# Optimization experiments

Measured on AMD Instinct MI355X. Metric: run time of the kernel, lower is better.

The kernel has to match this reference:

```python
import jax, jax.numpy as jnp
import numpy as np

# Product-key memory config (matches init_kwargs)
HEADS = 4
K_DIM = 512          # per-head query/key dim; split in two halves of 256
HALF = K_DIM // 2
V_DIM = 512
SUBSIZE = 512        # sub-keys per bank; value table size = SUBSIZE**2
SIZE = SUBSIZE * SUBSIZE
TOPK = 8
TEMP = 1.0
B, T = 4, 2048


def setup_inputs() -> dict:
    key = jax.random.key(0)
    kq, kk, kv = jax.random.split(key, 3)
    bound = 1.0 / np.sqrt(K_DIM)  # reset_parameters: uniform(-1/sqrt(k_dim), 1/sqrt(k_dim))
    query = jax.random.normal(kq, (B, T, HEADS * K_DIM), dtype=jnp.float32)
    keys = jax.random.uniform(kk, (2 * HEADS * SUBSIZE, HALF), dtype=jnp.float32,
                              minval=-bound, maxval=bound)
    # reset_parameters: normal(0, v_dim**-0.5)
    values = jax.random.normal(kv, (SIZE, V_DIM), dtype=jnp.float32) * (V_DIM ** -0.5)
    return {"query": query, "keys": keys, "values": values}


def reference(query, keys, values):
    """retrieve_values: product-key two-stage topk + softmax-weighted embedding bag.
    query: [B, T, HEADS*K_DIM]; keys: [2*HEADS*SUBSIZE, HALF]; values: [SIZE, V_DIM]
    returns retrieved values [B*T, V_DIM].
    """
    Bq, Tq = query.shape[:2]
    N = Bq * Tq
    q = query.reshape(N, HEADS, K_DIM)
    q1, q2 = q[..., :HALF], q[..., HALF:]
    k = keys.reshape(2, HEADS, SUBSIZE, HALF)

    # Sub-key score matmuls (the two 'cdist-like' searches)
    s1 = jnp.einsum('nhd,hsd->nhs', q1, k[0])       # [N, H, SUBSIZE]
    s2 = jnp.einsum('nhd,hsd->nhs', q2, k[1])       # [N, H, SUBSIZE]

    ts1, ti1 = jax.lax.top_k(s1, TOPK)               # [N, H, TOPK]
    ts2, ti2 = jax.lax.top_k(s2, TOPK)

    # Cartesian combination of the two topk sets, then global topk
    comb = (ts1[..., :, None] + ts2[..., None, :]).reshape(N, HEADS, TOPK * TOPK)
    scores, flat_idx = jax.lax.top_k(comb, TOPK)     # [N, H, TOPK]
    sel1 = jnp.take_along_axis(ti1, flat_idx // TOPK, axis=-1)
    sel2 = jnp.take_along_axis(ti2, flat_idx % TOPK, axis=-1)
    indices = sel1 * SUBSIZE + sel2                  # global value-table indices [N, H, TOPK]

    # score_transform: softmax over heads*topk (score_nonlinear='softmax')
    w = jax.nn.softmax(scores.reshape(N, HEADS * TOPK) / TEMP, axis=-1)

    # xformers_embedding_bag: weighted gather-sum over the huge value table
    gathered = values[indices.reshape(N, HEADS * TOPK)]   # [N, H*TOPK, V_DIM]
    vals = jnp.einsum('nk,nkd->nd', w, gathered)          # [N, V_DIM]
    return vals
```

## Files before the change

### kernel.cpp

```cpp
#include <hip/hip_runtime.h>
#include <hip/hip_bf16.h>
#include <math.h>

typedef unsigned short u16;
typedef __attribute__((ext_vector_type(8))) short short8;
typedef __attribute__((ext_vector_type(4))) float f32x4;

#define N_TOK   8192
#define N_HEADS 4
#define KDIM    512
#define HALFD   256
#define VDIM    512
#define SUBK    512
#define NCAND   16

__device__ __forceinline__ u16 f2bf(float f) {
    unsigned u = __float_as_uint(f);
    u += 0x7fffu + ((u >> 16) & 1u);
    return (u16)(u >> 16);
}

__device__ __forceinline__ unsigned med3u(unsigned a, unsigned b, unsigned c) {
    unsigned d;
    asm("v_med3_u32 %0, %1, %2, %3" : "=v"(d) : "v"(a), "v"(b), "v"(c));
    return d;
}

__global__ void k_convert(const float* __restrict__ in, u16* __restrict__ out, int n4) {
    int i = blockIdx.x * blockDim.x + threadIdx.x;
    int stride = gridDim.x * blockDim.x;
    for (; i < n4; i += stride) {
        float4 v = ((const float4*)in)[i];
        unsigned a = (unsigned)f2bf(v.x) | ((unsigned)f2bf(v.y) << 16);
        unsigned b = (unsigned)f2bf(v.z) | ((unsigned)f2bf(v.w) << 16);
        ((uint2*)out)[i] = make_uint2(a, b);
    }
}

__global__ __launch_bounds__(256) void k_score_topk(
    const float* __restrict__ query,
    const u16* __restrict__ kb,
    int* __restrict__ cand)
{
    __shared__ unsigned sc[16 * 513];
    const int nb = blockIdx.x, h = blockIdx.y, half = blockIdx.z;
    const int tid = threadIdx.x;
    const int wave = tid >> 6, l = tid & 63;
    const int lr = l & 15, lk = l >> 4;

    const float* qbase = query + (size_t)(nb * 16 + lr) * (N_HEADS * KDIM)
                       + h * KDIM + half * HALFD + lk * 8;
    short8 a[8];
#pragma unroll
    for (int kf = 0; kf < 8; ++kf) {
        float4 q0 = *(const float4*)(qbase + kf * 32);
        float4 q1 = *(const float4*)(qbase + kf * 32 + 4);
        short8 t;
        t[0] = (short)f2bf(q0.x); t[1] = (short)f2bf(q0.y);
        t[2] = (short)f2bf(q0.z); t[3] = (short)f2bf(q0.w);
        t[4] = (short)f2bf(q1.x); t[5] = (short)f2bf(q1.y);
        t[6] = (short)f2bf(q1.z); t[7] = (short)f2bf(q1.w);
        a[kf] = t;
    }

    const u16* kbase = kb + (size_t)(half * N_HEADS + h) * SUBK * HALFD;
#pragma unroll
    for (int t = 0; t < 8; ++t) {
        const int st = wave * 8 + t;
        const u16* kp = kbase + (size_t)(st * 16 + lr) * HALFD + lk * 8;
        short8 b[8];
#pragma unroll
        for (int kf = 0; kf < 8; ++kf)
            b[kf] = *(const short8*)(kp + kf * 32);
        f32x4 acc = {0.f, 0.f, 0.f, 0.f};
#pragma unroll
        for (int kf = 0; kf < 8; ++kf)
            acc = __builtin_amdgcn_mfma_f32_16x16x32_bf16(a[kf], b[kf], acc, 0, 0, 0);
#pragma unroll
        for (int r = 0; r < 4; ++r) {
            unsigned ub = __float_as_uint(acc[r]);
            unsigned key = ub ^ ((unsigned)((int)ub >> 31) | 0x80000000u);
            key = (key & 0xFFFFFE00u) | (unsigned)(st * 16 + lr);
            sc[(lk * 4 + r) * 513 + st * 16 + lr] = key;
        }
    }
    __syncthreads();

    const int row = tid >> 4, sub = tid & 15;
    unsigned tv[NCAND];
#pragma unroll
    for (int j = 0; j < NCAND; ++j) tv[j] = 0u;
    const int base = row * 513 + sub;
#pragma unroll
    for (int t = 0; t < 32; ++t) {
        unsigned v = sc[base + (t << 4)];
#pragma unroll
        for (int j = NCAND - 1; j >= 1; --j)
            tv[j] = med3u(tv[j - 1], tv[j], v);
        tv[0] = (tv[0] > v) ? tv[0] : v;
    }

    unsigned keep = 0;
#pragma unroll
    for (int r = 0; r < NCAND; ++r) {
        unsigned w = tv[0];
#pragma unroll
        for (int d = 1; d < 16; d <<= 1) {
            unsigned o = __shfl_xor(w, d, 16);
            w = (o > w) ? o : w;
        }
        if (sub == r) keep = w;
        bool pop = (tv[0] == w);
#pragma unroll
        for (int j = 0; j < NCAND - 1; ++j) tv[j] = pop ? tv[j + 1] : tv[j];
        tv[NCAND - 1] = pop ? 0u : tv[NCAND - 1];
    }
    const int n = nb * 16 + row;
    cand[((size_t)n * 8 + (h * 2 + half)) * NCAND + sub] = (int)(keep & 0x1FFu);
}

__global__ __launch_bounds__(256) void k_select(
    const float* __restrict__ query,
    const float* __restrict__ keys,
    const int* __restrict__ cand,
    int* __restrict__ gout,
    float* __restrict__ wout)
{
    __shared__ double rv[8][16];
    __shared__ int    ri[8][16];
    __shared__ double tsv[8][8];
    __shared__ int    tsi[8][8];
    __shared__ double s_comb[32];
    __shared__ int    sgi[32];

    const int n = blockIdx.x;
    const int tid = threadIdx.x;

    {
        const int dot = tid >> 1, pt = tid & 1;
        const int g = dot >> 4, j = dot & 15;
        const int h = g >> 1, half = g & 1;
        const int sidx = cand[((size_t)n * 8 + g) * NCAND + j];
        const float* qrow = query + (size_t)n * (N_HEADS * KDIM) + h * KDIM + half * HALFD + pt * 128;
        const float* krow = keys + ((size_t)(half * N_HEADS + h) * SUBK + sidx) * HALFD + pt * 128;
        double a0 = 0, a1 = 0, a2 = 0, a3 = 0;
#pragma unroll 8
        for (int d = 0; d < 128; d += 4) {
            float4 qv = *(const float4*)(qrow + d);
            float4 kv = *(const float4*)(krow + d);
            a0 = fma((double)qv.x, (double)kv.x, a0);
            a1 = fma((double)qv.y, (double)kv.y, a1);
            a2 = fma((double)qv.z, (double)kv.z, a2);
            a3 = fma((double)qv.w, (double)kv.w, a3);
        }
        double s = (a0 + a1) + (a2 + a3);
        double o = __shfl_xor(s, 1);
        if (pt == 0) { rv[g][j] = s + o; ri[g][j] = sidx; }
    }
    __syncthreads();

    if (tid < 128) {
        const int g = tid >> 4, j = tid & 15;
        double v = rv[g][j];
        const int idx = ri[g][j];
        for (int r = 0; r < 8; ++r) {
            double bv = v; int bj = j;
#pragma unroll
            for (int d = 1; d < 16; d <<= 1) {
                double ov = __shfl_xor(bv, d, 16);
                int    oj = __shfl_xor(bj, d, 16);
                if (ov > bv || (ov == bv && oj < bj)) { bv = ov; bj = oj; }
            }
            int widx = __shfl(idx, bj, 16);
            if (j == r) { tsv[g][r] = bv; tsi[g][r] = widx; }
            if (j == bj) v = -1e300;
        }
    }
    __syncthreads();

    {
        const int h = tid >> 6, f = tid & 63;
        double c = tsv[h * 2][f >> 3] + tsv[h * 2 + 1][f & 7];
        for (int r = 0; r < 8; ++r) {
            double bv = c; int bf = f;
#pragma unroll
            for (int d = 1; d < 64; d <<= 1) {
                double ov = __shfl_xor(bv, d, 64);
                int    of = __shfl_xor(bf, d, 64);
                if (ov > bv || (ov == bv && of < bf)) { bv = ov; bf = of; }
            }
            if (f == r) {
                s_comb[h * 8 + r] = bv;
                sgi[h * 8 + r] = tsi[h * 2][bf >> 3] * SUBK + tsi[h * 2 + 1][bf & 7];
            }
            if (f == bf) c = -1e300;
        }
    }
    __syncthreads();

    if (tid < 32) {
        const int k = tid;
        double s = s_comb[k];
        double m = s;
#pragma unroll
        for (int d = 1; d < 32; d <<= 1) m = fmax(m, __shfl_xor(m, d, 32));
        float e = expf((float)(s - m));
        float sum = e;
#pragma unroll
        for (int d = 1; d < 32; d <<= 1) sum += __shfl_xor(sum, d, 32);
        wout[(size_t)n * 32 + k] = e / sum;
        gout[(size_t)n * 32 + k] = sgi[k];
    }
}

__global__ __launch_bounds__(256) void k_gather(
    const float* __restrict__ values,
    const int* __restrict__ gidx,
    const float* __restrict__ w,
    float* __restrict__ out)
{
    const int tok = blockIdx.x * 4 + (threadIdx.x >> 6);
    const int lane = threadIdx.x & 63;

    float wv = 0.f; unsigned off = 0u;
    if (lane < 32) {
        wv  = w[(size_t)tok * 32 + lane];
        off = (unsigned)gidx[(size_t)tok * 32 + lane] * (unsigned)VDIM;
    }

    float4 acc0 = {0.f, 0.f, 0.f, 0.f};
    float4 acc1 = {0.f, 0.f, 0.f, 0.f};
#pragma unroll
    for (int kb = 0; kb < 32; kb += 8) {
        float4 v0[8], v1[8];
#pragma unroll
        for (int r = 0; r < 8; ++r) {
            unsigned o = (unsigned)__shfl((int)off, kb + r, 64);
            const float* vr = values + (size_t)o;
            v0[r] = *(const float4*)(vr + lane * 4);
            v1[r] = *(const float4*)(vr + 256 + lane * 4);
        }
#pragma unroll
        for (int r = 0; r < 8; ++r) {
            const float wk = __shfl(wv, kb + r, 64);
            acc0.x = fmaf(wk, v0[r].x, acc0.x);
            acc0.y = fmaf(wk, v0[r].y, acc0.y);
            acc0.z = fmaf(wk, v0[r].z, acc0.z);
            acc0.w = fmaf(wk, v0[r].w, acc0.w);
            acc1.x = fmaf(wk, v1[r].x, acc1.x);
            acc1.y = fmaf(wk, v1[r].y, acc1.y);
            acc1.z = fmaf(wk, v1[r].z, acc1.z);
            acc1.w = fmaf(wk, v1[r].w, acc1.w);
        }
    }
    float* orow = out + (size_t)tok * VDIM;
    *(float4*)(orow + lane * 4) = acc0;
    *(float4*)(orow + 256 + lane * 4) = acc1;
}

extern "C" void kernel_launch(void* const* d_in, const int* in_sizes, int n_in,
                              void* d_out, int out_size, void* d_ws, size_t ws_size,
                              hipStream_t stream) {
    const float* query  = (const float*)d_in[0];
    const float* keys   = (const float*)d_in[1];
    const float* values = (const float*)d_in[2];
    float* out = (float*)d_out;

    char* ws = (char*)d_ws;
    u16* kb    = (u16*)ws;
    int* cand  = (int*)(ws + 2097152);
    int* gidxb = (int*)(ws + 2097152 + 4194304);
    float* wb  = (float*)(ws + 2097152 + 4194304 + 1048576);

    k_convert<<<512, 256, 0, stream>>>(keys, kb, (2 * N_HEADS * SUBK * HALFD) / 4);

    dim3 gB(N_TOK / 16, N_HEADS, 2);
    k_score_topk<<<gB, 256, 0, stream>>>(query, kb, cand);

    k_select<<<N_TOK, 256, 0, stream>>>(query, keys, cand, gidxb, wb);
    k_gather<<<N_TOK / 4, 256, 0, stream>>>(values, gidxb, wb, out);
}
```

Measured before the change: 416.3 us.

## Process two tokens per wave and gather values in index-range passes

```diff
diff --git a/kernel.cpp b/kernel.cpp
--- a/kernel.cpp
+++ b/kernel.cpp
@@ -219,43 +219,57 @@
     const float* __restrict__ w,
     float* __restrict__ out)
 {
-    const int tok = blockIdx.x * 4 + (threadIdx.x >> 6);
+    const int wid = blockIdx.x * 4 + (threadIdx.x >> 6);
     const int lane = threadIdx.x & 63;
-
-    float wv = 0.f; unsigned off = 0u;
+    const int t0 = wid * 2, t1 = t0 + 1;
+
+    float wv0 = 0.f, wv1 = 0.f;
+    unsigned r0 = 0xFFFFFFFFu, r1 = 0xFFFFFFFFu;
     if (lane < 32) {
-        wv  = w[(size_t)tok * 32 + lane];
-        off = (unsigned)gidx[(size_t)tok * 32 + lane] * (unsigned)VDIM;
-    }
-
-    float4 acc0 = {0.f, 0.f, 0.f, 0.f};
-    float4 acc1 = {0.f, 0.f, 0.f, 0.f};
-#pragma unroll
-    for (int kb = 0; kb < 32; kb += 8) {
-        float4 v0[8], v1[8];
-#pragma unroll
-        for (int r = 0; r < 8; ++r) {
-            unsigned o = (unsigned)__shfl((int)off, kb + r, 64);
-            const float* vr = values + (size_t)o;
-            v0[r] = *(const float4*)(vr + lane * 4);
-            v1[r] = *(const float4*)(vr + 256 + lane * 4);
-        }
-#pragma unroll
-        for (int r = 0; r < 8; ++r) {
-            const float wk = __shfl(wv, kb + r, 64);
-            acc0.x = fmaf(wk, v0[r].x, acc0.x);
-            acc0.y = fmaf(wk, v0[r].y, acc0.y);
-            acc0.z = fmaf(wk, v0[r].z, acc0.z);
-            acc0.w = fmaf(wk, v0[r].w, acc0.w);
-            acc1.x = fmaf(wk, v1[r].x, acc1.x);
-            acc1.y = fmaf(wk, v1[r].y, acc1.y);
-            acc1.z = fmaf(wk, v1[r].z, acc1.z);
-            acc1.w = fmaf(wk, v1[r].w, acc1.w);
-        }
-    }
-    float* orow = out + (size_t)tok * VDIM;
-    *(float4*)(orow + lane * 4) = acc0;
-    *(float4*)(orow + 256 + lane * 4) = acc1;
+        wv0 = w[(size_t)t0 * 32 + lane];
+        r0  = (unsigned)gidx[(size_t)t0 * 32 + lane];
+        wv1 = w[(size_t)t1 * 32 + lane];
+        r1  = (unsigned)gidx[(size_t)t1 * 32 + lane];
+    }
+
+    float4 a00 = {0,0,0,0}, a01 = {0,0,0,0};
+    float4 a10 = {0,0,0,0}, a11 = {0,0,0,0};
+
+    for (unsigned s = 0; s < 4; ++s) {
+        for (int k = 0; k < 32; ++k) {
+            unsigned o = (unsigned)__shfl((int)r0, k, 64);
+            if ((o >> 16) == s) {
+                const float* vr = values + (size_t)o * VDIM;
+                float4 v0 = *(const float4*)(vr + lane * 4);
+                float4 v1 = *(const float4*)(vr + 256 + lane * 4);
+                const float wk = __shfl(wv0, k, 64);
+                a00.x = fmaf(wk, v0.x, a00.x); a00.y = fmaf(wk, v0.y, a00.y);
+                a00.z = fmaf(wk, v0.z, a00.z); a00.w = fmaf(wk, v0.w, a00.w);
+                a01.x = fmaf(wk, v1.x, a01.x); a01.y = fmaf(wk, v1.y, a01.y);
+                a01.z = fmaf(wk, v1.z, a01.z); a01.w = fmaf(wk, v1.w, a01.w);
+            }
+        }
+        for (int k = 0; k < 32; ++k) {
+            unsigned o = (unsigned)__shfl((int)r1, k, 64);
+            if ((o >> 16) == s) {
+                const float* vr = values + (size_t)o * VDIM;
+                float4 v0 = *(const float4*)(vr + lane * 4);
+                float4 v1 = *(const float4*)(vr + 256 + lane * 4);
+                const float wk = __shfl(wv1, k, 64);
+                a10.x = fmaf(wk, v0.x, a10.x); a10.y = fmaf(wk, v0.y, a10.y);
+                a10.z = fmaf(wk, v0.z, a10.z); a10.w = fmaf(wk, v0.w, a10.w);
+                a11.x = fmaf(wk, v1.x, a11.x); a11.y = fmaf(wk, v1.y, a11.y);
+                a11.z = fmaf(wk, v1.z, a11.z); a11.w = fmaf(wk, v1.w, a11.w);
+            }
+        }
+    }
+
+    float* o0 = out + (size_t)t0 * VDIM;
+    *(float4*)(o0 + lane * 4) = a00;
+    *(float4*)(o0 + 256 + lane * 4) = a01;
+    float* o1 = out + (size_t)t1 * VDIM;
+    *(float4*)(o1 + lane * 4) = a10;
+    *(float4*)(o1 + 256 + lane * 4) = a11;
 }
 
 extern "C" void kernel_launch(void* const* d_in, const int* in_sizes, int n_in,
@@ -278,5 +292,5 @@
     k_score_topk<<<gB, 256, 0, stream>>>(query, kb, cand);
 
     k_select<<<N_TOK, 256, 0, stream>>>(query, keys, cand, gidxb, wb);
-    k_gather<<<N_TOK / 4, 256, 0, stream>>>(values, gidxb, wb, out);
-}
+    k_gather<<<1024, 256, 0, stream>>>(values, gidxb, wb, out);
+}
```

New measurement: 412.7 us. About the same (-0.9%).
